# Optimization experiments

Measured on AMD Instinct MI355X. Metric: run time of the kernel, lower is better.

Reference implementation:

```python
import jax, jax.numpy as jnp
import numpy as np

N, E, B = 50000, 600000, 64
C_IN, H, C_OUT, L = 128, 128, 64, 3
BN_EPS = 1e-5


def setup_inputs() -> dict:
    key = jax.random.key(0)
    ks = iter(jax.random.split(key, 40))

    def w(shape, fan_in):
        return jax.random.normal(next(ks), shape, jnp.float32) / np.sqrt(fan_in).astype(np.float32)

    return {
        "x": jax.random.normal(next(ks), (N, C_IN), jnp.float32),
        "edge_index": jax.random.randint(next(ks), (2, E), 0, N),
        "batch": jnp.sort(jax.random.randint(next(ks), (N,), 0, B)),
        # GINConv MLPs: Linear(in,h) -> BN -> ReLU -> Linear(h,h)   (stacked over L; C_IN == H)
        "convW1": w((L, C_IN, H), C_IN), "convb1": jnp.zeros((L, H), jnp.float32),
        "bn_g": jnp.ones((L, H), jnp.float32), "bn_b": jnp.zeros((L, H), jnp.float32),
        "convW2": w((L, H, H), H), "convb2": jnp.zeros((L, H), jnp.float32),
        # reconstruction head: Linear(h,h)-ReLU-Linear(h,h)-ReLU-Linear(h,4)-ReLU
        "recW1": w((H, H), H), "recb1": jnp.zeros((H,), jnp.float32),
        "recW2": w((H, H), H), "recb2": jnp.zeros((H,), jnp.float32),
        "recW3": w((H, 4), H), "recb3": jnp.zeros((4,), jnp.float32),
        # final MLP([h,h,out], norm=None): Linear(h,h)-ReLU-(dropout, eval=identity)-Linear(h,out)
        "mlpW1": w((H, H), H), "mlpb1": jnp.zeros((H,), jnp.float32),
        "mlpW2": w((H, C_OUT), H), "mlpb2": jnp.zeros((C_OUT,), jnp.float32),
    }


def reference(x, edge_index, batch, convW1, convb1, bn_g, bn_b, convW2, convb2,
              recW1, recb1, recW2, recb2, recW3, recb3, mlpW1, mlpb1, mlpW2, mlpb2):
    src, dst = edge_index[0], edge_index[1]
    for l in range(L):
        # GIN aggregation: out_i = nn((1+eps)*x_i + sum_{j->i} x_j), eps = 0
        agg = jax.ops.segment_sum(x[src], dst, num_segments=N)  # [N, d]
        h = (x + agg) @ convW1[l] + convb1[l]                   # [N, H]
        mu = h.mean(axis=0)
        var = jnp.var(h, axis=0)                                # biased, torch BN train mode
        h = bn_g[l] * (h - mu) * jax.lax.rsqrt(var + BN_EPS) + bn_b[l]
        h = jax.nn.relu(h) @ convW2[l] + convb2[l]
        x = jax.nn.relu(h)                                      # outer .relu() in forward
    # reconstruction branch on node features
    x_rec = jax.nn.relu(x @ recW1 + recb1)
    x_rec = jax.nn.relu(x_rec @ recW2 + recb2)
    x_rec = jax.nn.relu(x_rec @ recW3 + recb3)                  # [N, 4]
    # global_add_pool keyed by graph id
    pooled = jax.ops.segment_sum(x, batch, num_segments=B)      # [B, H]
    out = jax.nn.relu(pooled @ mlpW1 + mlpb1) @ mlpW2 + mlpb2   # [B, C_OUT]
    return (out, x_rec)
```

## Files before the change

kernel.cpp:

```cpp
#include <hip/hip_runtime.h>

#define NN 50000
#define EE 600000
#define BB 64
#define CH 128
#define LL 3
#define NGB 391
#define NSB 196
#define NPB 392

typedef unsigned short u16;
typedef unsigned int u32;
typedef short s16x8 __attribute__((ext_vector_type(8)));
typedef float f32x4 __attribute__((ext_vector_type(4)));

__device__ __forceinline__ u16 f2b(float f) {
    u32 x = __float_as_uint(f);
    return (u16)((x + 0x7FFFu + ((x >> 16) & 1u)) >> 16);
}
__device__ __forceinline__ float b2f(u16 u) {
    return __uint_as_float(((u32)u) << 16);
}

__global__ __launch_bounds__(256) void k_zero2(int* __restrict__ deg,
                                               float* __restrict__ pooled,
                                               float* __restrict__ gstats,
                                               int* __restrict__ bar) {
    int i = blockIdx.x * 256 + threadIdx.x;
    if (i < NN) deg[i] = 0;
    int j = i - NN;
    if (j >= 0 && j < BB * CH) pooled[j] = 0.f;
    int k = j - BB * CH;
    if (k >= 0 && k < 3 * 256) gstats[k] = 0.f;
    int l = k - 3 * 256;
    if (l >= 0 && l < 4) bar[l] = 0;
}

__global__ __launch_bounds__(256) void k_count(const int* __restrict__ ei,
                                               int* __restrict__ deg) {
    int e = blockIdx.x * 256 + threadIdx.x;
    if (e < EE) atomicAdd(&deg[ei[EE + e]], 1);
}

__global__ __launch_bounds__(256) void k_scanA(const int* __restrict__ deg,
                                               int* __restrict__ bsum) {
    __shared__ int sm[256];
    int i = blockIdx.x * 256 + threadIdx.x;
    sm[threadIdx.x] = (i < NN) ? deg[i] : 0;
    __syncthreads();
    for (int off = 128; off > 0; off >>= 1) {
        if (threadIdx.x < off) sm[threadIdx.x] += sm[threadIdx.x + off];
        __syncthreads();
    }
    if (threadIdx.x == 0) bsum[blockIdx.x] = sm[0];
}

__global__ __launch_bounds__(256) void k_scanB(const int* __restrict__ deg,
                                               const int* __restrict__ bsum,
                                               int* __restrict__ rowptr,
                                               int* __restrict__ cur) {
    __shared__ int sb[256], sd[256];
    int t = threadIdx.x;
    sb[t] = (t < NSB) ? bsum[t] : 0;
    __syncthreads();
    for (int off = 1; off < 256; off <<= 1) {
        int v = (t >= off) ? sb[t - off] : 0;
        __syncthreads();
        sb[t] += v;
        __syncthreads();
    }
    int blockOff = (blockIdx.x == 0) ? 0 : sb[blockIdx.x - 1];
    int i = blockIdx.x * 256 + t;
    int d = (i < NN) ? deg[i] : 0;
    sd[t] = d;
    __syncthreads();
    for (int off = 1; off < 256; off <<= 1) {
        int v = (t >= off) ? sd[t - off] : 0;
        __syncthreads();
        sd[t] += v;
        __syncthreads();
    }
    int excl = blockOff + sd[t] - d;
    if (i < NN) { rowptr[i] = excl; cur[i] = excl; }
    if (i == NN - 1) rowptr[NN] = excl + d;
}

__global__ __launch_bounds__(256) void k_fill(const int* __restrict__ ei,
                                              int* __restrict__ cur,
                                              int* __restrict__ perm) {
    int e = blockIdx.x * 256 + threadIdx.x;
    if (e < EE) {
        int dst = ei[EE + e];
        int idx = atomicAdd(&cur[dst], 1);
        perm[idx] = ei[e];
    }
}

__global__ __launch_bounds__(256) void k_cvt(const float* __restrict__ x,
                                             u16* __restrict__ y) {
    long base = (long)(blockIdx.x * 256 + threadIdx.x) * 8;
    if (base < (long)NN * CH) {
        float4 f0 = *(const float4*)(x + base);
        float4 f1 = *(const float4*)(x + base + 4);
        union { u16 pk[8]; uint4 v; } uu;
        uu.pk[0] = f2b(f0.x); uu.pk[1] = f2b(f0.y);
        uu.pk[2] = f2b(f0.z); uu.pk[3] = f2b(f0.w);
        uu.pk[4] = f2b(f1.x); uu.pk[5] = f2b(f1.y);
        uu.pk[6] = f2b(f1.z); uu.pk[7] = f2b(f1.w);
        *(uint4*)(y + base) = uu.v;
    }
}

__global__ __launch_bounds__(256) void k_gather(const u16* __restrict__ x,
                                                const int* __restrict__ rowptr,
                                                const int* __restrict__ perm,
                                                u16* __restrict__ y) {
    int dst = blockIdx.x * 16 + (threadIdx.x >> 4);
    if (dst >= NN) return;
    int lane = threadIdx.x & 15;
    int co = lane * 8;
    int beg = rowptr[dst], end = rowptr[dst + 1];
    union { u16 pk[8]; uint4 v; } uu;
    uu.v = *(const uint4*)(x + (long)dst * CH + co);
    float a[8], b[8];
#pragma unroll
    for (int j = 0; j < 8; ++j) { a[j] = b2f(uu.pk[j]); b[j] = 0.f; }
    int e = beg;
    for (; e + 1 < end; e += 2) {
        int s0 = perm[e], s1 = perm[e + 1];
        union { u16 pk[8]; uint4 v; } v0, v1;
        v0.v = *(const uint4*)(x + (long)s0 * CH + co);
        v1.v = *(const uint4*)(x + (long)s1 * CH + co);
#pragma unroll
        for (int j = 0; j < 8; ++j) { a[j] += b2f(v0.pk[j]); b[j] += b2f(v1.pk[j]); }
    }
    if (e < end) {
        int s0 = perm[e];
        union { u16 pk[8]; uint4 v; } v0;
        v0.v = *(const uint4*)(x + (long)s0 * CH + co);
#pragma unroll
        for (int j = 0; j < 8; ++j) a[j] += b2f(v0.pk[j]);
    }
    union { u16 pk[8]; uint4 v; } ov;
#pragma unroll
    for (int j = 0; j < 8; ++j) ov.pk[j] = f2b(a[j] + b[j]);
    *(uint4*)(y + (long)dst * CH + co) = ov.v;
}

__global__ __launch_bounds__(256) void k_transpose_all(
    const float* __restrict__ cW1, const float* __restrict__ cW2,
    const float* __restrict__ rW1, const float* __restrict__ rW2,
    const float* __restrict__ rW3, u16* __restrict__ Wt) {
    int idx = blockIdx.x * 256 + threadIdx.x;
    if (idx < 8 * 16384) {
        int slot = idx >> 14;
        int wi = idx & 16383;
        int k = wi >> 7, n = wi & 127;
        const float* src = slot < 3 ? cW1 + slot * 16384
                         : slot < 6 ? cW2 + (slot - 3) * 16384
                         : slot == 6 ? rW1 : rW2;
        Wt[slot * 16384 + n * 128 + k] = f2b(src[wi]);
    } else if (idx < 9 * 16384) {
        int j = idx - 8 * 16384;
        int n = j >> 7, k = j & 127;
        Wt[8 * 16384 + j] = (n < 4) ? f2b(rW3[k * 4 + n]) : (u16)0;
    }
}

__device__ __forceinline__ void stageB8(const u16* __restrict__ Wt, u16* sB,
                                        int s, int rr) {
#pragma unroll
    for (int it = 0; it < 8; ++it) {
        int n = it * 16 + rr;
        uint4 u = *(const uint4*)(Wt + n * CH + 8 * s);
        *(uint4*)(&sB[n * CH + ((s ^ (n & 15)) * 8)]) = u;
    }
}

__device__ __forceinline__ void mfma8(const u16* sA, const u16* sB,
                                      f32x4 acc[2][8], int wv, int quad, int l16) {
    f32x4 z = {0.f, 0.f, 0.f, 0.f};
#pragma unroll
    for (int m = 0; m < 2; ++m)
#pragma unroll
        for (int t = 0; t < 8; ++t) acc[m][t] = z;
    const u16* pa0 = sA + (wv * 32 + l16) * CH;
    const u16* pa1 = pa0 + 16 * CH;
#pragma unroll
    for (int kc = 0; kc < 4; ++kc) {
        int off = (((kc << 2) | quad) ^ l16) << 3;
        s16x8 a0 = *(const s16x8*)(pa0 + off);
        s16x8 a1 = *(const s16x8*)(pa1 + off);
#pragma unroll
        for (int t = 0; t < 8; ++t) {
            s16x8 bfr = *(const s16x8*)(sB + (t * 16 + l16) * CH + off);
            acc[0][t] = __builtin_amdgcn_mfma_f32_16x16x32_bf16(a0, bfr, acc[0][t], 0, 0, 0);
            acc[1][t] = __builtin_amdgcn_mfma_f32_16x16x32_bf16(a1, bfr, acc[1][t], 0, 0, 0);
        }
    }
}

__device__ __forceinline__ void biasrelu(f32x4 acc[2][8],
                                         const float* __restrict__ bias, int l16) {
#pragma unroll
    for (int t = 0; t < 8; ++t) {
        float bv = bias[t * 16 + l16];
#pragma unroll
        for (int m = 0; m < 2; ++m)
#pragma unroll
            for (int r = 0; r < 4; ++r)
                acc[m][t][r] = fmaxf(acc[m][t][r] + bv, 0.f);
    }
}

__device__ __forceinline__ void restage(const f32x4 acc[2][8], u16* sA,
                                        int wv, int quad, int l16) {
#pragma unroll
    for (int t = 0; t < 8; ++t) {
        int chunk = (t << 1) | (l16 >> 3);
        int o7 = l16 & 7;
#pragma unroll
        for (int m = 0; m < 2; ++m)
#pragma unroll
            for (int r = 0; r < 4; ++r) {
                int lr = wv * 32 + m * 16 + quad * 4 + r;
                sA[lr * CH + ((chunk ^ (lr & 15)) << 3) + o7] = f2b(acc[m][t][r]);
            }
    }
}

__device__ __forceinline__ void grid_barrier(int* bar, int tid) {
    __syncthreads();
    if (tid == 0) {
        __hip_atomic_fetch_add(bar, 1, __ATOMIC_RELEASE, __HIP_MEMORY_SCOPE_AGENT);
        while (__hip_atomic_load(bar, __ATOMIC_RELAXED, __HIP_MEMORY_SCOPE_AGENT) < NGB) {
            __builtin_amdgcn_s_sleep(2);
        }
        (void)__hip_atomic_load(bar, __ATOMIC_ACQUIRE, __HIP_MEMORY_SCOPE_AGENT);
    }
    __syncthreads();
}

template <bool LAST>
__global__ __launch_bounds__(256, 2) void k_layer(
    const u16* __restrict__ y16, const u16* __restrict__ Wt, int layer,
    const float* __restrict__ cb1, const float* __restrict__ cb2,
    const float* __restrict__ g, const float* __restrict__ bbeta,
    float* __restrict__ gstats, int* __restrict__ bar, u16* __restrict__ xc,
    const float* __restrict__ rb1, const float* __restrict__ rb2,
    const float* __restrict__ rb3, float* __restrict__ x_rec) {
    __shared__ u16 sA[128 * CH];
    __shared__ u16 sB[128 * CH];
    const int tid = threadIdx.x;
    const int s = tid & 15, rr = tid >> 4;
    const int r0 = blockIdx.x * 128;
    const int lane = tid & 63, wv = tid >> 6, quad = lane >> 4, l16 = lane & 15;

    stageB8(Wt + layer * 16384, sB, s, rr);
#pragma unroll
    for (int it = 0; it < 8; ++it) {
        int lr = it * 16 + rr, gr = r0 + lr;
        union { u16 pk[8]; uint4 v; } uu;
        if (gr < NN) {
            uu.v = *(const uint4*)(y16 + (long)gr * CH + 8 * s);
        } else {
#pragma unroll
            for (int j = 0; j < 8; ++j) uu.pk[j] = 0;
        }
        *(uint4*)(&sA[lr * CH + ((s ^ (lr & 15)) * 8)]) = uu.v;
    }
    __syncthreads();
    f32x4 acc[2][8];
    mfma8(sA, sB, acc, wv, quad, l16);

    float ss[8], qq[8];
#pragma unroll
    for (int t = 0; t < 8; ++t) {
        float bv = cb1[t * 16 + l16];
        ss[t] = 0.f; qq[t] = 0.f;
#pragma unroll
        for (int m = 0; m < 2; ++m) {
            int rbase = r0 + wv * 32 + m * 16 + quad * 4;
#pragma unroll
            for (int r = 0; r < 4; ++r) {
                float v = acc[m][t][r] + bv;
                acc[m][t][r] = v;
                if (rbase + r < NN) { ss[t] += v; qq[t] += v * v; }
            }
        }
    }
#pragma unroll
    for (int t = 0; t < 8; ++t) {
        ss[t] += __shfl_xor(ss[t], 16);
        ss[t] += __shfl_xor(ss[t], 32);
        qq[t] += __shfl_xor(qq[t], 16);
        qq[t] += __shfl_xor(qq[t], 32);
    }
    float* red = (float*)sA;
    __syncthreads();
    if (lane < 16) {
#pragma unroll
        for (int t = 0; t < 8; ++t) {
            red[wv * 256 + t * 16 + l16] = ss[t];
            red[wv * 256 + 128 + t * 16 + l16] = qq[t];
        }
    }
    __syncthreads();
    unsafeAtomicAdd(&gstats[tid],
                    red[tid] + red[256 + tid] + red[512 + tid] + red[768 + tid]);

    stageB8(Wt + (3 + layer) * 16384, sB, s, rr);

    grid_barrier(bar, tid);

#pragma unroll
    for (int t = 0; t < 8; ++t) {
        int col = t * 16 + l16;
        float sum = __hip_atomic_load(&gstats[col], __ATOMIC_RELAXED,
                                      __HIP_MEMORY_SCOPE_AGENT);
        float sq = __hip_atomic_load(&gstats[128 + col], __ATOMIC_RELAXED,
                                     __HIP_MEMORY_SCOPE_AGENT);
        float mu = sum / (float)NN;
        float var = sq / (float)NN - mu * mu;
        float rstd = rsqrtf(var + 1e-5f);
        float sc = g[col] * rstd;
        float sh = bbeta[col] - mu * sc;
#pragma unroll
        for (int m = 0; m < 2; ++m)
#pragma unroll
            for (int r = 0; r < 4; ++r)
                acc[m][t][r] = fmaxf(acc[m][t][r] * sc + sh, 0.f);
    }

    restage(acc, sA, wv, quad, l16);
    __syncthreads();
    mfma8(sA, sB, acc, wv, quad, l16);
    biasrelu(acc, cb2, l16);
#pragma unroll
    for (int t = 0; t < 8; ++t) {
        int col = t * 16 + l16;
#pragma unroll
        for (int m = 0; m < 2; ++m)
#pragma unroll
            for (int r = 0; r < 4; ++r) {
                int row = r0 + wv * 32 + m * 16 + quad * 4 + r;
                if (row < NN) xc[(long)row * CH + col] = f2b(acc[m][t][r]);
            }
    }

    if constexpr (LAST) {
        __syncthreads();
        restage(acc, sA, wv, quad, l16);
        stageB8(Wt + 6 * 16384, sB, s, rr);
        __syncthreads();
        mfma8(sA, sB, acc, wv, quad, l16);
        biasrelu(acc, rb1, l16);
        __syncthreads();
        restage(acc, sA, wv, quad, l16);
        stageB8(Wt + 7 * 16384, sB, s, rr);
        __syncthreads();
        mfma8(sA, sB, acc, wv, quad, l16);
        biasrelu(acc, rb2, l16);
        __syncthreads();
        restage(acc, sA, wv, quad, l16);
        {
            int n = rr;
            uint4 u = *(const uint4*)(Wt + 8 * 16384 + n * CH + 8 * s);
            *(uint4*)(&sB[n * CH + ((s ^ (n & 15)) * 8)]) = u;
        }
        __syncthreads();
        f32x4 a4[2];
        a4[0] = (f32x4){0.f, 0.f, 0.f, 0.f};
        a4[1] = (f32x4){0.f, 0.f, 0.f, 0.f};
        const u16* pa0 = sA + (wv * 32 + l16) * CH;
        const u16* pa1 = pa0 + 16 * CH;
#pragma unroll
        for (int kc = 0; kc < 4; ++kc) {
            int off = (((kc << 2) | quad) ^ l16) << 3;
            s16x8 a0 = *(const s16x8*)(pa0 + off);
            s16x8 a1 = *(const s16x8*)(pa1 + off);
            s16x8 bfr = *(const s16x8*)(sB + l16 * CH + off);
            a4[0] = __builtin_amdgcn_mfma_f32_16x16x32_bf16(a0, bfr, a4[0], 0, 0, 0);
            a4[1] = __builtin_amdgcn_mfma_f32_16x16x32_bf16(a1, bfr, a4[1], 0, 0, 0);
        }
        if (l16 < 4) {
            float bv = rb3[l16];
#pragma unroll
            for (int m = 0; m < 2; ++m)
#pragma unroll
                for (int r = 0; r < 4; ++r) {
                    int row = r0 + wv * 32 + m * 16 + quad * 4 + r;
                    if (row < NN) x_rec[(long)row * 4 + l16] = fmaxf(a4[m][r] + bv, 0.f);
                }
        }
    }
}

__global__ __launch_bounds__(256) void k_pool(const u16* __restrict__ x,
                                              const int* __restrict__ batch,
                                              float* __restrict__ pooled) {
    int r0 = blockIdx.x * 128;
    if (r0 >= NN) return;
    int rend = r0 + 128 < NN ? r0 + 128 : NN;
    int c = threadIdx.x & 127;
    int half = threadIdx.x >> 7;
    int r = r0 + half;
    if (r >= rend) return;
    int g = batch[r];
    float s = 0.f;
    for (; r < rend; r += 2) {
        int gg = batch[r];
        if (gg != g) {
            unsafeAtomicAdd(pooled + g * CH + c, s);
            s = 0.f;
            g = gg;
        }
        s += b2f(x[(long)r * CH + c]);
    }
    unsafeAtomicAdd(pooled + g * CH + c, s);
}

__global__ __launch_bounds__(128) void k_mlp(const float* __restrict__ pooled,
                                             const float* __restrict__ W1,
                                             const float* __restrict__ b1,
                                             const float* __restrict__ W2,
                                             const float* __restrict__ b2,
                                             float* __restrict__ out) {
    __shared__ float p[128], t1[128];
    int b = blockIdx.x, t = threadIdx.x;
    p[t] = pooled[b * CH + t];
    __syncthreads();
    float acc = b1[t];
    for (int k = 0; k < 128; ++k) acc += p[k] * W1[k * 128 + t];
    t1[t] = fmaxf(acc, 0.f);
    __syncthreads();
    if (t < 64) {
        float o = b2[t];
        for (int k = 0; k < 128; ++k) o += t1[k] * W2[k * 64 + t];
        out[b * 64 + t] = o;
    }
}

extern "C" void kernel_launch(void* const* d_in, const int* in_sizes, int n_in,
                              void* d_out, int out_size, void* d_ws, size_t ws_size,
                              hipStream_t stream) {
    const float* x_in   = (const float*)d_in[0];
    const int*   ei     = (const int*)d_in[1];
    const int*   batch  = (const int*)d_in[2];
    const float* convW1 = (const float*)d_in[3];
    const float* convb1 = (const float*)d_in[4];
    const float* bn_g   = (const float*)d_in[5];
    const float* bn_b   = (const float*)d_in[6];
    const float* convW2 = (const float*)d_in[7];
    const float* convb2 = (const float*)d_in[8];
    const float* recW1  = (const float*)d_in[9];
    const float* recb1  = (const float*)d_in[10];
    const float* recW2  = (const float*)d_in[11];
    const float* recb2  = (const float*)d_in[12];
    const float* recW3  = (const float*)d_in[13];
    const float* recb3  = (const float*)d_in[14];
    const float* mlpW1  = (const float*)d_in[15];
    const float* mlpb1  = (const float*)d_in[16];
    const float* mlpW2  = (const float*)d_in[17];
    const float* mlpb2  = (const float*)d_in[18];

    float* out   = (float*)d_out;
    float* x_rec = out + 4096;

    char* w = (char*)d_ws;
    u16*   x16    = (u16*)w;    w += (size_t)NN * CH * 2;
    u16*   y16    = (u16*)w;    w += (size_t)NN * CH * 2;
    u16*   xc     = (u16*)w;    w += (size_t)NN * CH * 2;
    u16*   Wt     = (u16*)w;    w += (size_t)9 * 16384 * 2;
    float* gstats = (float*)w;  w += (size_t)3 * 256 * 4;
    int*   bar    = (int*)w;    w += 4 * 4;
    float* pooled = (float*)w;  w += (size_t)BB * CH * 4;
    int*   deg    = (int*)w;    w += (size_t)NN * 4;
    int*   bsum   = (int*)w;    w += (size_t)NSB * 4;
    int*   rowptr = (int*)w;    w += (size_t)(NN + 1) * 4;
    int*   cur    = (int*)w;    w += (size_t)NN * 4;
    int*   perm   = (int*)w;    w += (size_t)EE * 4;

    dim3 b256(256), b128(128);

    k_zero2<<<231, b256, 0, stream>>>(deg, pooled, gstats, bar);
    k_count<<<2344, b256, 0, stream>>>(ei, deg);
    k_scanA<<<NSB, b256, 0, stream>>>(deg, bsum);
    k_scanB<<<NSB, b256, 0, stream>>>(deg, bsum, rowptr, cur);
    k_fill<<<2344, b256, 0, stream>>>(ei, cur, perm);
    k_cvt<<<3125, b256, 0, stream>>>(x_in, x16);
    k_transpose_all<<<576, b256, 0, stream>>>(convW1, convW2, recW1, recW2, recW3, Wt);

    const u16* cur_x = x16;
    for (int l = 0; l < LL; ++l) {
        k_gather<<<3125, b256, 0, stream>>>(cur_x, rowptr, perm, y16);
        if (l < LL - 1)
            k_layer<false><<<NGB, b256, 0, stream>>>(
                y16, Wt, l, convb1 + l * 128, convb2 + l * 128,
                bn_g + l * 128, bn_b + l * 128, gstats + l * 256, bar + l, xc,
                recb1, recb2, recb3, x_rec);
        else
            k_layer<true><<<NGB, b256, 0, stream>>>(
                y16, Wt, l, convb1 + l * 128, convb2 + l * 128,
                bn_g + l * 128, bn_b + l * 128, gstats + l * 256, bar + l, xc,
                recb1, recb2, recb3, x_rec);
        cur_x = xc;
    }
    k_pool<<<NPB, b256, 0, stream>>>(xc, batch, pooled);
    k_mlp<<<64, b128, 0, stream>>>(pooled, mlpW1, mlpb1, mlpW2, mlpb2, out);
}
```

Measured before the change: 440.0 us.

## Halve weight LDS buffer and stage weights in two halves for occupancy

Shrinks the shared-memory weight tile from 128 to 64 output columns and runs each 128x128 GEMM as two passes, restaging the second half of the weights between them. The launch bound goes from two to three blocks per CU so more blocks can be resident, which matters for the persistent grid-barrier kernel. The cost is extra __syncthreads and a second weight load from global or L2 per GEMM. Tighter register limits could also cause spills.

After: 434.2 us. About the same (-1.3%).

```diff
diff --git a/kernel.cpp b/kernel.cpp
--- a/kernel.cpp
+++ b/kernel.cpp
@@ -167,23 +167,19 @@
     }
 }
 
-__device__ __forceinline__ void stageB8(const u16* __restrict__ Wt, u16* sB,
+__device__ __forceinline__ void stageB4(const u16* __restrict__ Wt, u16* sB,
                                         int s, int rr) {
 #pragma unroll
-    for (int it = 0; it < 8; ++it) {
+    for (int it = 0; it < 4; ++it) {
         int n = it * 16 + rr;
         uint4 u = *(const uint4*)(Wt + n * CH + 8 * s);
         *(uint4*)(&sB[n * CH + ((s ^ (n & 15)) * 8)]) = u;
     }
 }
 
-__device__ __forceinline__ void mfma8(const u16* sA, const u16* sB,
-                                      f32x4 acc[2][8], int wv, int quad, int l16) {
-    f32x4 z = {0.f, 0.f, 0.f, 0.f};
-#pragma unroll
-    for (int m = 0; m < 2; ++m)
-#pragma unroll
-        for (int t = 0; t < 8; ++t) acc[m][t] = z;
+__device__ __forceinline__ void mfma4(const u16* sA, const u16* sB,
+                                      f32x4* acc0, f32x4* acc1,
+                                      int wv, int quad, int l16) {
     const u16* pa0 = sA + (wv * 32 + l16) * CH;
     const u16* pa1 = pa0 + 16 * CH;
 #pragma unroll
@@ -192,10 +188,10 @@
         s16x8 a0 = *(const s16x8*)(pa0 + off);
         s16x8 a1 = *(const s16x8*)(pa1 + off);
 #pragma unroll
-        for (int t = 0; t < 8; ++t) {
+        for (int t = 0; t < 4; ++t) {
             s16x8 bfr = *(const s16x8*)(sB + (t * 16 + l16) * CH + off);
-            acc[0][t] = __builtin_amdgcn_mfma_f32_16x16x32_bf16(a0, bfr, acc[0][t], 0, 0, 0);
-            acc[1][t] = __builtin_amdgcn_mfma_f32_16x16x32_bf16(a1, bfr, acc[1][t], 0, 0, 0);
+            acc0[t] = __builtin_amdgcn_mfma_f32_16x16x32_bf16(a0, bfr, acc0[t], 0, 0, 0);
+            acc1[t] = __builtin_amdgcn_mfma_f32_16x16x32_bf16(a1, bfr, acc1[t], 0, 0, 0);
         }
     }
 }
@@ -229,6 +225,25 @@
     }
 }
 
+template <bool PRE0>
+__device__ __forceinline__ void gemm_halves(const u16* sA, u16* sB,
+                                            const u16* __restrict__ Wt,
+                                            f32x4 acc[2][8],
+                                            int s, int rr, int wv, int quad, int l16) {
+    f32x4 z = {0.f, 0.f, 0.f, 0.f};
+#pragma unroll
+    for (int m = 0; m < 2; ++m)
+#pragma unroll
+        for (int t = 0; t < 8; ++t) acc[m][t] = z;
+    if constexpr (PRE0) stageB4(Wt, sB, s, rr);
+    __syncthreads();
+    mfma4(sA, sB, &acc[0][0], &acc[1][0], wv, quad, l16);
+    __syncthreads();
+    stageB4(Wt + 64 * CH, sB, s, rr);
+    __syncthreads();
+    mfma4(sA, sB, &acc[0][4], &acc[1][4], wv, quad, l16);
+}
+
 __device__ __forceinline__ void grid_barrier(int* bar, int tid) {
     __syncthreads();
     if (tid == 0) {
@@ -242,7 +257,7 @@
 }
 
 template <bool LAST>
-__global__ __launch_bounds__(256, 2) void k_layer(
+__global__ __launch_bounds__(256, 3) void k_layer(
     const u16* __restrict__ y16, const u16* __restrict__ Wt, int layer,
     const float* __restrict__ cb1, const float* __restrict__ cb2,
     const float* __restrict__ g, const float* __restrict__ bbeta,
@@ -250,13 +265,12 @@
     const float* __restrict__ rb1, const float* __restrict__ rb2,
     const float* __restrict__ rb3, float* __restrict__ x_rec) {
     __shared__ u16 sA[128 * CH];
-    __shared__ u16 sB[128 * CH];
+    __shared__ u16 sB[64 * CH];
     const int tid = threadIdx.x;
     const int s = tid & 15, rr = tid >> 4;
     const int r0 = blockIdx.x * 128;
     const int lane = tid & 63, wv = tid >> 6, quad = lane >> 4, l16 = lane & 15;
 
-    stageB8(Wt + layer * 16384, sB, s, rr);
 #pragma unroll
     for (int it = 0; it < 8; ++it) {
         int lr = it * 16 + rr, gr = r0 + lr;
@@ -269,9 +283,8 @@
         }
         *(uint4*)(&sA[lr * CH + ((s ^ (lr & 15)) * 8)]) = uu.v;
     }
-    __syncthreads();
     f32x4 acc[2][8];
-    mfma8(sA, sB, acc, wv, quad, l16);
+    gemm_halves<true>(sA, sB, Wt + layer * 16384, acc, s, rr, wv, quad, l16);
 
     float ss[8], qq[8];
 #pragma unroll
@@ -309,7 +322,7 @@
     unsafeAtomicAdd(&gstats[tid],
                     red[tid] + red[256 + tid] + red[512 + tid] + red[768 + tid]);
 
-    stageB8(Wt + (3 + layer) * 16384, sB, s, rr);
+    stageB4(Wt + (3 + layer) * 16384, sB, s, rr);
 
     grid_barrier(bar, tid);
 
@@ -333,8 +346,7 @@
     }
 
     restage(acc, sA, wv, quad, l16);
-    __syncthreads();
-    mfma8(sA, sB, acc, wv, quad, l16);
+    gemm_halves<false>(sA, sB, Wt + (3 + layer) * 16384, acc, s, rr, wv, quad, l16);
     biasrelu(acc, cb2, l16);
 #pragma unroll
     for (int t = 0; t < 8; ++t) {
@@ -349,20 +361,17 @@
     }
 
     if constexpr (LAST) {
+        f32x4 nacc[2][8];
         __syncthreads();
         restage(acc, sA, wv, quad, l16);
-        stageB8(Wt + 6 * 16384, sB, s, rr);
-        __syncthreads();
-        mfma8(sA, sB, acc, wv, quad, l16);
-        biasrelu(acc, rb1, l16);
-        __syncthreads();
-        restage(acc, sA, wv, quad, l16);
-        stageB8(Wt + 7 * 16384, sB, s, rr);
-        __syncthreads();
-        mfma8(sA, sB, acc, wv, quad, l16);
-        biasrelu(acc, rb2, l16);
-        __syncthreads();
-        restage(acc, sA, wv, quad, l16);
+        gemm_halves<true>(sA, sB, Wt + 6 * 16384, nacc, s, rr, wv, quad, l16);
+        biasrelu(nacc, rb1, l16);
+        __syncthreads();
+        restage(nacc, sA, wv, quad, l16);
+        gemm_halves<true>(sA, sB, Wt + 7 * 16384, nacc, s, rr, wv, quad, l16);
+        biasrelu(nacc, rb2, l16);
+        __syncthreads();
+        restage(nacc, sA, wv, quad, l16);
         {
             int n = rr;
             uint4 u = *(const uint4*)(Wt + 8 * 16384 + n * CH + 8 * s);
```

## Fuse neighbor gather into first GEMM and replace grid barrier with split kernels

Applied to the files above, without the earlier changes.

Moves the GIN neighbor aggregation into the first-linear kernel, so gathered rows go straight into shared memory instead of through a global buffer. The persistent layer kernel and its spin-wait grid barrier are replaced by three launches: a first GEMM that also accumulates BN statistics, a tiny kernel that computes BN scale and shift, and a second GEMM that applies BN and ReLU on load. Row tiles shrink from 128 to 64 and the grid doubles, so more blocks can be resident. In exchange, the pre-BN activation is written to and read back from global memory in bf16, and each layer adds one extra launch.

After: 506.9 us. 1.15x slower.

```diff
diff --git a/kernel.cpp b/kernel.cpp
--- a/kernel.cpp
+++ b/kernel.cpp
@@ -5,7 +5,7 @@
 #define BB 64
 #define CH 128
 #define LL 3
-#define NGB 391
+#define NGB 782
 #define NSB 196
 #define NPB 392
 
@@ -24,16 +24,13 @@
 
 __global__ __launch_bounds__(256) void k_zero2(int* __restrict__ deg,
                                                float* __restrict__ pooled,
-                                               float* __restrict__ gstats,
-                                               int* __restrict__ bar) {
+                                               float* __restrict__ gstats) {
     int i = blockIdx.x * 256 + threadIdx.x;
     if (i < NN) deg[i] = 0;
     int j = i - NN;
     if (j >= 0 && j < BB * CH) pooled[j] = 0.f;
     int k = j - BB * CH;
     if (k >= 0 && k < 3 * 256) gstats[k] = 0.f;
-    int l = k - 3 * 256;
-    if (l >= 0 && l < 4) bar[l] = 0;
 }
 
 __global__ __launch_bounds__(256) void k_count(const int* __restrict__ ei,
@@ -109,42 +106,6 @@
         uu.pk[6] = f2b(f1.z); uu.pk[7] = f2b(f1.w);
         *(uint4*)(y + base) = uu.v;
     }
-}
-
-__global__ __launch_bounds__(256) void k_gather(const u16* __restrict__ x,
-                                                const int* __restrict__ rowptr,
-                                                const int* __restrict__ perm,
-                                                u16* __restrict__ y) {
-    int dst = blockIdx.x * 16 + (threadIdx.x >> 4);
-    if (dst >= NN) return;
-    int lane = threadIdx.x & 15;
-    int co = lane * 8;
-    int beg = rowptr[dst], end = rowptr[dst + 1];
-    union { u16 pk[8]; uint4 v; } uu;
-    uu.v = *(const uint4*)(x + (long)dst * CH + co);
-    float a[8], b[8];
-#pragma unroll
-    for (int j = 0; j < 8; ++j) { a[j] = b2f(uu.pk[j]); b[j] = 0.f; }
-    int e = beg;
-    for (; e + 1 < end; e += 2) {
-        int s0 = perm[e], s1 = perm[e + 1];
-        union { u16 pk[8]; uint4 v; } v0, v1;
-        v0.v = *(const uint4*)(x + (long)s0 * CH + co);
-        v1.v = *(const uint4*)(x + (long)s1 * CH + co);
-#pragma unroll
-        for (int j = 0; j < 8; ++j) { a[j] += b2f(v0.pk[j]); b[j] += b2f(v1.pk[j]); }
-    }
-    if (e < end) {
-        int s0 = perm[e];
-        union { u16 pk[8]; uint4 v; } v0;
-        v0.v = *(const uint4*)(x + (long)s0 * CH + co);
-#pragma unroll
-        for (int j = 0; j < 8; ++j) a[j] += b2f(v0.pk[j]);
-    }
-    union { u16 pk[8]; uint4 v; } ov;
-#pragma unroll
-    for (int j = 0; j < 8; ++j) ov.pk[j] = f2b(a[j] + b[j]);
-    *(uint4*)(y + (long)dst * CH + co) = ov.v;
 }
 
 __global__ __launch_bounds__(256) void k_transpose_all(
@@ -177,115 +138,122 @@
     }
 }
 
-__device__ __forceinline__ void mfma8(const u16* sA, const u16* sB,
-                                      f32x4 acc[2][8], int wv, int quad, int l16) {
+__device__ __forceinline__ void mfma64(const u16* sA, const u16* sB,
+                                       f32x4 acc[8], int wv, int quad, int l16) {
     f32x4 z = {0.f, 0.f, 0.f, 0.f};
 #pragma unroll
-    for (int m = 0; m < 2; ++m)
-#pragma unroll
-        for (int t = 0; t < 8; ++t) acc[m][t] = z;
-    const u16* pa0 = sA + (wv * 32 + l16) * CH;
-    const u16* pa1 = pa0 + 16 * CH;
+    for (int t = 0; t < 8; ++t) acc[t] = z;
+    const u16* pa = sA + (wv * 16 + l16) * CH;
 #pragma unroll
     for (int kc = 0; kc < 4; ++kc) {
         int off = (((kc << 2) | quad) ^ l16) << 3;
-        s16x8 a0 = *(const s16x8*)(pa0 + off);
-        s16x8 a1 = *(const s16x8*)(pa1 + off);
+        s16x8 a0 = *(const s16x8*)(pa + off);
 #pragma unroll
         for (int t = 0; t < 8; ++t) {
             s16x8 bfr = *(const s16x8*)(sB + (t * 16 + l16) * CH + off);
-            acc[0][t] = __builtin_amdgcn_mfma_f32_16x16x32_bf16(a0, bfr, acc[0][t], 0, 0, 0);
-            acc[1][t] = __builtin_amdgcn_mfma_f32_16x16x32_bf16(a1, bfr, acc[1][t], 0, 0, 0);
-        }
-    }
-}
-
-__device__ __forceinline__ void biasrelu(f32x4 acc[2][8],
-                                         const float* __restrict__ bias, int l16) {
+            acc[t] = __builtin_amdgcn_mfma_f32_16x16x32_bf16(a0, bfr, acc[t], 0, 0, 0);
+        }
+    }
+}
+
+__device__ __forceinline__ void biasrelu64(f32x4 acc[8],
+                                           const float* __restrict__ bias, int l16) {
 #pragma unroll
     for (int t = 0; t < 8; ++t) {
         float bv = bias[t * 16 + l16];
 #pragma unroll
-        for (int m = 0; m < 2; ++m)
-#pragma unroll
-            for (int r = 0; r < 4; ++r)
-                acc[m][t][r] = fmaxf(acc[m][t][r] + bv, 0.f);
-    }
-}
-
-__device__ __forceinline__ void restage(const f32x4 acc[2][8], u16* sA,
-                                        int wv, int quad, int l16) {
+        for (int r = 0; r < 4; ++r)
+            acc[t][r] = fmaxf(acc[t][r] + bv, 0.f);
+    }
+}
+
+__device__ __forceinline__ void restage64(const f32x4 acc[8], u16* sA,
+                                          int wv, int quad, int l16) {
 #pragma unroll
     for (int t = 0; t < 8; ++t) {
         int chunk = (t << 1) | (l16 >> 3);
         int o7 = l16 & 7;
 #pragma unroll
-        for (int m = 0; m < 2; ++m)
-#pragma unroll
-            for (int r = 0; r < 4; ++r) {
-                int lr = wv * 32 + m * 16 + quad * 4 + r;
-                sA[lr * CH + ((chunk ^ (lr & 15)) << 3) + o7] = f2b(acc[m][t][r]);
+        for (int r = 0; r < 4; ++r) {
+            int lr = wv * 16 + quad * 4 + r;
+            sA[lr * CH + ((chunk ^ (lr & 15)) << 3) + o7] = f2b(acc[t][r]);
+        }
+    }
+}
+
+__device__ __forceinline__ void gatherA(const u16* __restrict__ x,
+                                        const int* __restrict__ rowptr,
+                                        const int* __restrict__ perm,
+                                        u16* sA, int r0, int s, int rr) {
+#pragma unroll
+    for (int j = 0; j < 4; ++j) {
+        int lr = rr * 4 + j;
+        int gr = r0 + lr;
+        union { u16 pk[8]; uint4 v; } uu;
+        if (gr < NN) {
+            uu.v = *(const uint4*)(x + (long)gr * CH + 8 * s);
+            float a[8], b[8];
+#pragma unroll
+            for (int q = 0; q < 8; ++q) { a[q] = b2f(uu.pk[q]); b[q] = 0.f; }
+            int e = rowptr[gr], end = rowptr[gr + 1];
+            for (; e + 1 < end; e += 2) {
+                int s0 = perm[e], s1 = perm[e + 1];
+                union { u16 pk[8]; uint4 v; } v0, v1;
+                v0.v = *(const uint4*)(x + (long)s0 * CH + 8 * s);
+                v1.v = *(const uint4*)(x + (long)s1 * CH + 8 * s);
+#pragma unroll
+                for (int q = 0; q < 8; ++q) { a[q] += b2f(v0.pk[q]); b[q] += b2f(v1.pk[q]); }
             }
-    }
-}
-
-__device__ __forceinline__ void grid_barrier(int* bar, int tid) {
-    __syncthreads();
-    if (tid == 0) {
-        __hip_atomic_fetch_add(bar, 1, __ATOMIC_RELEASE, __HIP_MEMORY_SCOPE_AGENT);
-        while (__hip_atomic_load(bar, __ATOMIC_RELAXED, __HIP_MEMORY_SCOPE_AGENT) < NGB) {
-            __builtin_amdgcn_s_sleep(2);
-        }
-        (void)__hip_atomic_load(bar, __ATOMIC_ACQUIRE, __HIP_MEMORY_SCOPE_AGENT);
-    }
-    __syncthreads();
-}
-
-template <bool LAST>
-__global__ __launch_bounds__(256, 2) void k_layer(
-    const u16* __restrict__ y16, const u16* __restrict__ Wt, int layer,
-    const float* __restrict__ cb1, const float* __restrict__ cb2,
-    const float* __restrict__ g, const float* __restrict__ bbeta,
-    float* __restrict__ gstats, int* __restrict__ bar, u16* __restrict__ xc,
-    const float* __restrict__ rb1, const float* __restrict__ rb2,
-    const float* __restrict__ rb3, float* __restrict__ x_rec) {
-    __shared__ u16 sA[128 * CH];
+            if (e < end) {
+                int s0 = perm[e];
+                union { u16 pk[8]; uint4 v; } v0;
+                v0.v = *(const uint4*)(x + (long)s0 * CH + 8 * s);
+#pragma unroll
+                for (int q = 0; q < 8; ++q) a[q] += b2f(v0.pk[q]);
+            }
+#pragma unroll
+            for (int q = 0; q < 8; ++q) uu.pk[q] = f2b(a[q] + b[q]);
+        } else {
+#pragma unroll
+            for (int q = 0; q < 8; ++q) uu.pk[q] = 0;
+        }
+        *(uint4*)(&sA[lr * CH + ((s ^ (lr & 15)) * 8)]) = uu.v;
+    }
+}
+
+__global__ __launch_bounds__(256, 3) void k_g1(
+    const u16* __restrict__ x, const int* __restrict__ rowptr,
+    const int* __restrict__ perm, const u16* __restrict__ Wt1,
+    const float* __restrict__ cb1, u16* __restrict__ h16,
+    float* __restrict__ gstats) {
+    __shared__ u16 sA[64 * CH];
     __shared__ u16 sB[128 * CH];
     const int tid = threadIdx.x;
     const int s = tid & 15, rr = tid >> 4;
-    const int r0 = blockIdx.x * 128;
+    const int r0 = blockIdx.x * 64;
     const int lane = tid & 63, wv = tid >> 6, quad = lane >> 4, l16 = lane & 15;
 
-    stageB8(Wt + layer * 16384, sB, s, rr);
-#pragma unroll
-    for (int it = 0; it < 8; ++it) {
-        int lr = it * 16 + rr, gr = r0 + lr;
-        union { u16 pk[8]; uint4 v; } uu;
-        if (gr < NN) {
-            uu.v = *(const uint4*)(y16 + (long)gr * CH + 8 * s);
-        } else {
-#pragma unroll
-            for (int j = 0; j < 8; ++j) uu.pk[j] = 0;
-        }
-        *(uint4*)(&sA[lr * CH + ((s ^ (lr & 15)) * 8)]) = uu.v;
-    }
-    __syncthreads();
-    f32x4 acc[2][8];
-    mfma8(sA, sB, acc, wv, quad, l16);
+    stageB8(Wt1, sB, s, rr);
+    gatherA(x, rowptr, perm, sA, r0, s, rr);
+    __syncthreads();
+
+    f32x4 acc[8];
+    mfma64(sA, sB, acc, wv, quad, l16);
 
     float ss[8], qq[8];
 #pragma unroll
     for (int t = 0; t < 8; ++t) {
         float bv = cb1[t * 16 + l16];
+        int col = t * 16 + l16;
         ss[t] = 0.f; qq[t] = 0.f;
-#pragma unroll
-        for (int m = 0; m < 2; ++m) {
-            int rbase = r0 + wv * 32 + m * 16 + quad * 4;
-#pragma unroll
-            for (int r = 0; r < 4; ++r) {
-                float v = acc[m][t][r] + bv;
-                acc[m][t][r] = v;
-                if (rbase + r < NN) { ss[t] += v; qq[t] += v * v; }
+        int rbase = r0 + wv * 16 + quad * 4;
+#pragma unroll
+        for (int r = 0; r < 4; ++r) {
+            float v = acc[t][r] + bv;
+            int row = rbase + r;
+            if (row < NN) {
+                ss[t] += v; qq[t] += v * v;
+                h16[(long)row * CH + col] = f2b(v);
             }
         }
     }
@@ -308,90 +276,156 @@
     __syncthreads();
     unsafeAtomicAdd(&gstats[tid],
                     red[tid] + red[256 + tid] + red[512 + tid] + red[768 + tid]);
-
-    stageB8(Wt + (3 + layer) * 16384, sB, s, rr);
-
-    grid_barrier(bar, tid);
-
+}
+
+__global__ __launch_bounds__(128) void k_bnparam(const float* __restrict__ gstats,
+                                                 const float* __restrict__ g,
+                                                 const float* __restrict__ b,
+                                                 float* __restrict__ scale,
+                                                 float* __restrict__ shift) {
+    int t = threadIdx.x;
+    float mu = gstats[t] / (float)NN;
+    float var = gstats[128 + t] / (float)NN - mu * mu;
+    float rstd = rsqrtf(var + 1e-5f);
+    float sc = g[t] * rstd;
+    scale[t] = sc;
+    shift[t] = b[t] - mu * sc;
+}
+
+__global__ __launch_bounds__(256, 3) void k_g2(
+    const u16* __restrict__ h16, const u16* __restrict__ Wt2,
+    const float* __restrict__ cb2, const float* __restrict__ scale,
+    const float* __restrict__ shift, u16* __restrict__ xc) {
+    __shared__ u16 sA[64 * CH];
+    __shared__ u16 sB[128 * CH];
+    const int tid = threadIdx.x;
+    const int s = tid & 15, rr = tid >> 4;
+    const int r0 = blockIdx.x * 64;
+    const int lane = tid & 63, wv = tid >> 6, quad = lane >> 4, l16 = lane & 15;
+
+    float sc[8], sh[8];
+#pragma unroll
+    for (int j = 0; j < 8; ++j) { sc[j] = scale[8 * s + j]; sh[j] = shift[8 * s + j]; }
+
+    stageB8(Wt2, sB, s, rr);
+#pragma unroll
+    for (int it = 0; it < 4; ++it) {
+        int lr = it * 16 + rr;
+        int gr = r0 + lr;
+        union { u16 pk[8]; uint4 v; } uu;
+        if (gr < NN) {
+            uu.v = *(const uint4*)(h16 + (long)gr * CH + 8 * s);
+#pragma unroll
+            for (int j = 0; j < 8; ++j)
+                uu.pk[j] = f2b(fmaxf(b2f(uu.pk[j]) * sc[j] + sh[j], 0.f));
+        } else {
+#pragma unroll
+            for (int j = 0; j < 8; ++j) uu.pk[j] = 0;
+        }
+        *(uint4*)(&sA[lr * CH + ((s ^ (lr & 15)) * 8)]) = uu.v;
+    }
+    __syncthreads();
+
+    f32x4 acc[8];
+    mfma64(sA, sB, acc, wv, quad, l16);
+    biasrelu64(acc, cb2, l16);
 #pragma unroll
     for (int t = 0; t < 8; ++t) {
         int col = t * 16 + l16;
-        float sum = __hip_atomic_load(&gstats[col], __ATOMIC_RELAXED,
-                                      __HIP_MEMORY_SCOPE_AGENT);
-        float sq = __hip_atomic_load(&gstats[128 + col], __ATOMIC_RELAXED,
-                                     __HIP_MEMORY_SCOPE_AGENT);
-        float mu = sum / (float)NN;
-        float var = sq / (float)NN - mu * mu;
-        float rstd = rsqrtf(var + 1e-5f);
-        float sc = g[col] * rstd;
-        float sh = bbeta[col] - mu * sc;
-#pragma unroll
-        for (int m = 0; m < 2; ++m)
-#pragma unroll
-            for (int r = 0; r < 4; ++r)
-                acc[m][t][r] = fmaxf(acc[m][t][r] * sc + sh, 0.f);
-    }
-
-    restage(acc, sA, wv, quad, l16);
-    __syncthreads();
-    mfma8(sA, sB, acc, wv, quad, l16);
-    biasrelu(acc, cb2, l16);
+        int rbase = r0 + wv * 16 + quad * 4;
+#pragma unroll
+        for (int r = 0; r < 4; ++r) {
+            int row = rbase + r;
+            if (row < NN) xc[(long)row * CH + col] = f2b(acc[t][r]);
+        }
+    }
+}
+
+__global__ __launch_bounds__(256, 3) void k_tail(
+    const u16* __restrict__ h16, const u16* __restrict__ Wt,
+    const float* __restrict__ cb2, const float* __restrict__ scale,
+    const float* __restrict__ shift, const float* __restrict__ rb1,
+    const float* __restrict__ rb2, const float* __restrict__ rb3,
+    u16* __restrict__ xc, float* __restrict__ x_rec) {
+    __shared__ u16 sA[64 * CH];
+    __shared__ u16 sB[128 * CH];
+    const int tid = threadIdx.x;
+    const int s = tid & 15, rr = tid >> 4;
+    const int r0 = blockIdx.x * 64;
+    const int lane = tid & 63, wv = tid >> 6, quad = lane >> 4, l16 = lane & 15;
+
+    float sc[8], sh[8];
+#pragma unroll
+    for (int j = 0; j < 8; ++j) { sc[j] = scale[8 * s + j]; sh[j] = shift[8 * s + j]; }
+
+    stageB8(Wt + 5 * 16384, sB, s, rr);
+#pragma unroll
+    for (int it = 0; it < 4; ++it) {
+        int lr = it * 16 + rr;
+        int gr = r0 + lr;
+        union { u16 pk[8]; uint4 v; } uu;
+        if (gr < NN) {
+            uu.v = *(const uint4*)(h16 + (long)gr * CH + 8 * s);
+#pragma unroll
+            for (int j = 0; j < 8; ++j)
+                uu.pk[j] = f2b(fmaxf(b2f(uu.pk[j]) * sc[j] + sh[j], 0.f));
+        } else {
+#pragma unroll
+            for (int j = 0; j < 8; ++j) uu.pk[j] = 0;
+        }
+        *(uint4*)(&sA[lr * CH + ((s ^ (lr & 15)) * 8)]) = uu.v;
+    }
+    __syncthreads();
+
+    f32x4 acc[8];
+    mfma64(sA, sB, acc, wv, quad, l16);
+    biasrelu64(acc, cb2, l16);
 #pragma unroll
     for (int t = 0; t < 8; ++t) {
         int col = t * 16 + l16;
-#pragma unroll
-        for (int m = 0; m < 2; ++m)
-#pragma unroll
-            for (int r = 0; r < 4; ++r) {
-                int row = r0 + wv * 32 + m * 16 + quad * 4 + r;
-                if (row < NN) xc[(long)row * CH + col] = f2b(acc[m][t][r]);
-            }
-    }
-
-    if constexpr (LAST) {
-        __syncthreads();
-        restage(acc, sA, wv, quad, l16);
-        stageB8(Wt + 6 * 16384, sB, s, rr);
-        __syncthreads();
-        mfma8(sA, sB, acc, wv, quad, l16);
-        biasrelu(acc, rb1, l16);
-        __syncthreads();
-        restage(acc, sA, wv, quad, l16);
-        stageB8(Wt + 7 * 16384, sB, s, rr);
-        __syncthreads();
-        mfma8(sA, sB, acc, wv, quad, l16);
-        biasrelu(acc, rb2, l16);
-        __syncthreads();
-        restage(acc, sA, wv, quad, l16);
-        {
-            int n = rr;
-            uint4 u = *(const uint4*)(Wt + 8 * 16384 + n * CH + 8 * s);
-            *(uint4*)(&sB[n * CH + ((s ^ (n & 15)) * 8)]) = u;
-        }
-        __syncthreads();
-        f32x4 a4[2];
-        a4[0] = (f32x4){0.f, 0.f, 0.f, 0.f};
-        a4[1] = (f32x4){0.f, 0.f, 0.f, 0.f};
-        const u16* pa0 = sA + (wv * 32 + l16) * CH;
-        const u16* pa1 = pa0 + 16 * CH;
-#pragma unroll
-        for (int kc = 0; kc < 4; ++kc) {
-            int off = (((kc << 2) | quad) ^ l16) << 3;
-            s16x8 a0 = *(const s16x8*)(pa0 + off);
-            s16x8 a1 = *(const s16x8*)(pa1 + off);
-            s16x8 bfr = *(const s16x8*)(sB + l16 * CH + off);
-            a4[0] = __builtin_amdgcn_mfma_f32_16x16x32_bf16(a0, bfr, a4[0], 0, 0, 0);
-            a4[1] = __builtin_amdgcn_mfma_f32_16x16x32_bf16(a1, bfr, a4[1], 0, 0, 0);
-        }
-        if (l16 < 4) {
-            float bv = rb3[l16];
-#pragma unroll
-            for (int m = 0; m < 2; ++m)
-#pragma unroll
-                for (int r = 0; r < 4; ++r) {
-                    int row = r0 + wv * 32 + m * 16 + quad * 4 + r;
-                    if (row < NN) x_rec[(long)row * 4 + l16] = fmaxf(a4[m][r] + bv, 0.f);
-                }
+        int rbase = r0 + wv * 16 + quad * 4;
+#pragma unroll
+        for (int r = 0; r < 4; ++r) {
+            int row = rbase + r;
+            if (row < NN) xc[(long)row * CH + col] = f2b(acc[t][r]);
+        }
+    }
+    __syncthreads();
+    restage64(acc, sA, wv, quad, l16);
+    stageB8(Wt + 6 * 16384, sB, s, rr);
+    __syncthreads();
+    mfma64(sA, sB, acc, wv, quad, l16);
+    biasrelu64(acc, rb1, l16);
+    __syncthreads();
+    restage64(acc, sA, wv, quad, l16);
+    stageB8(Wt + 7 * 16384, sB, s, rr);
+    __syncthreads();
+    mfma64(sA, sB, acc, wv, quad, l16);
+    biasrelu64(acc, rb2, l16);
+    __syncthreads();
+    restage64(acc, sA, wv, quad, l16);
+    {
+        int n = rr;
+        uint4 u = *(const uint4*)(Wt + 8 * 16384 + n * CH + 8 * s);
+        *(uint4*)(&sB[n * CH + ((s ^ (n & 15)) * 8)]) = u;
+    }
+    __syncthreads();
+    f32x4 a4 = {0.f, 0.f, 0.f, 0.f};
+    const u16* pa = sA + (wv * 16 + l16) * CH;
+#pragma unroll
+    for (int kc = 0; kc < 4; ++kc) {
+        int off = (((kc << 2) | quad) ^ l16) << 3;
+        s16x8 a0 = *(const s16x8*)(pa + off);
+        s16x8 bfr = *(const s16x8*)(sB + l16 * CH + off);
+        a4 = __builtin_amdgcn_mfma_f32_16x16x32_bf16(a0, bfr, a4, 0, 0, 0);
+    }
+    if (l16 < 4) {
+        float bv = rb3[l16];
+        int rbase = r0 + wv * 16 + quad * 4;
+#pragma unroll
+        for (int r = 0; r < 4; ++r) {
+            int row = rbase + r;
+            if (row < NN) x_rec[(long)row * 4 + l16] = fmaxf(a4[r] + bv, 0.f);
         }
     }
 }
@@ -469,11 +503,12 @@
 
     char* w = (char*)d_ws;
     u16*   x16    = (u16*)w;    w += (size_t)NN * CH * 2;
-    u16*   y16    = (u16*)w;    w += (size_t)NN * CH * 2;
+    u16*   h16    = (u16*)w;    w += (size_t)NN * CH * 2;
     u16*   xc     = (u16*)w;    w += (size_t)NN * CH * 2;
     u16*   Wt     = (u16*)w;    w += (size_t)9 * 16384 * 2;
     float* gstats = (float*)w;  w += (size_t)3 * 256 * 4;
-    int*   bar    = (int*)w;    w += 4 * 4;
+    float* scale  = (float*)w;  w += 128 * 4;
+    float* shift  = (float*)w;  w += 128 * 4;
     float* pooled = (float*)w;  w += (size_t)BB * CH * 4;
     int*   deg    = (int*)w;    w += (size_t)NN * 4;
     int*   bsum   = (int*)w;    w += (size_t)NSB * 4;
@@ -483,7 +518,7 @@
 
     dim3 b256(256), b128(128);
 
-    k_zero2<<<231, b256, 0, stream>>>(deg, pooled, gstats, bar);
+    k_zero2<<<231, b256, 0, stream>>>(deg, pooled, gstats);
     k_count<<<2344, b256, 0, stream>>>(ei, deg);
     k_scanA<<<NSB, b256, 0, stream>>>(deg, bsum);
     k_scanB<<<NSB, b256, 0, stream>>>(deg, bsum, rowptr, cur);
@@ -493,17 +528,16 @@
 
     const u16* cur_x = x16;
     for (int l = 0; l < LL; ++l) {
-        k_gather<<<3125, b256, 0, stream>>>(cur_x, rowptr, perm, y16);
+        k_g1<<<NGB, b256, 0, stream>>>(cur_x, rowptr, perm, Wt + l * 16384,
+                                       convb1 + l * 128, h16, gstats + l * 256);
+        k_bnparam<<<1, b128, 0, stream>>>(gstats + l * 256, bn_g + l * 128,
+                                          bn_b + l * 128, scale, shift);
         if (l < LL - 1)
-            k_layer<false><<<NGB, b256, 0, stream>>>(
-                y16, Wt, l, convb1 + l * 128, convb2 + l * 128,
-                bn_g + l * 128, bn_b + l * 128, gstats + l * 256, bar + l, xc,
-                recb1, recb2, recb3, x_rec);
+            k_g2<<<NGB, b256, 0, stream>>>(h16, Wt + (3 + l) * 16384,
+                                           convb2 + l * 128, scale, shift, xc);
         else
-            k_layer<true><<<NGB, b256, 0, stream>>>(
-                y16, Wt, l, convb1 + l * 128, convb2 + l * 128,
-                bn_g + l * 128, bn_b + l * 128, gstats + l * 256, bar + l, xc,
-                recb1, recb2, recb3, x_rec);
+            k_tail<<<NGB, b256, 0, stream>>>(h16, Wt, convb2 + 2 * 128, scale, shift,
+                                             recb1, recb2, recb3, xc, x_rec);
         cur_x = xc;
     }
     k_pool<<<NPB, b256, 0, stream>>>(xc, batch, pooled);
```
